# Optimization experiments

Measured on AMD Instinct MI355X. Metric: run time of the kernel, lower is better.

Reference implementation:

```python
import jax, jax.numpy as jnp
import numpy as np

NUM_NODES = 200000
NUM_EDGES = 4000000
NUM_GRAPHS = 512
D = 20
OUT = 5


def setup_inputs() -> dict:
    key = jax.random.key(0)
    k1, k2, k3, k4, k5, k6, k7 = jax.random.split(key, 7)
    x = jax.random.normal(k1, (NUM_NODES, D), dtype=jnp.float32)
    edge_index = jax.random.randint(k2, (2, NUM_EDGES), 0, NUM_NODES, dtype=jnp.int64)
    batch = jnp.sort(jax.random.randint(k3, (NUM_NODES,), 0, NUM_GRAPHS, dtype=jnp.int64))
    # GCNConv weight (glorot-ish) and bias; Linear(20 -> 5) weight/bias
    W1 = jax.random.normal(k4, (D, D), dtype=jnp.float32) / np.sqrt(D)
    b1 = jnp.zeros((D,), dtype=jnp.float32)
    W_out = jax.random.normal(k5, (D, OUT), dtype=jnp.float32) / np.sqrt(D)
    b_out = jax.random.normal(k6, (OUT,), dtype=jnp.float32) * 0.01
    return {"x": x, "edge_index": edge_index, "batch": batch,
            "W1": W1, "b1": b1, "W_out": W_out, "b_out": b_out}


def gcn_conv(x, edge_index, W, b, num_nodes):
    # PyG GCNConv: add self-loops, symmetric norm, linear transform, scatter-add, bias
    loop = jnp.arange(num_nodes, dtype=edge_index.dtype)
    src = jnp.concatenate([edge_index[0], loop])
    dst = jnp.concatenate([edge_index[1], loop])
    deg = jax.ops.segment_sum(jnp.ones_like(dst, dtype=x.dtype), dst, num_segments=num_nodes)
    dinv = jnp.where(deg > 0, jax.lax.rsqrt(deg), 0.0)
    norm = dinv[src] * dinv[dst]  # [E+N]
    h = x @ W                      # [N, D] transform first (cheaper than per-edge)
    msg = h[src] * norm[:, None]   # gather + scale  [E+N, D]
    out = jax.ops.segment_sum(msg, dst, num_segments=num_nodes)  # scatter-add
    return out + b


def reference(x, edge_index, batch, W1, b1, W_out, b_out):
    h = gcn_conv(x, edge_index, W1, b1, NUM_NODES)
    h = jax.nn.relu(h)
    # global mean pool per graph
    sums = jax.ops.segment_sum(h, batch, num_segments=NUM_GRAPHS)          # [G, D]
    cnts = jax.ops.segment_sum(jnp.ones((h.shape[0],), h.dtype), batch, num_segments=NUM_GRAPHS)
    pooled = sums / jnp.maximum(cnts, 1.0)[:, None]
    logits = pooled @ W_out + b_out                                        # [G, 5]
    return jax.nn.softmax(logits, axis=-1)
```

## Files before the change

kernel.cpp:

```cpp
#include <hip/hip_runtime.h>
#include <hip/hip_fp16.h>

#define N_NODES 200000
#define N_EDGES 4000000
#define N_GRAPHS 512
#define D 20
#define OUT 5

#define BSH 6
#define BN 64
#define NFB 3125
#define NFBP 3136
#define NCB 49
#define NC 500
#define CHUNK 8000
#define CH2 7168
#define NCH2 13
#define MAX_EB 1792
#define GMAX 8

__launch_bounds__(1024)
__global__ void k_hist(const int* __restrict__ dst, int* __restrict__ hist_g,
                       float* __restrict__ gsum, int* __restrict__ bucket_tot) {
    __shared__ int h[NFBP];
    int t = threadIdx.x;
    if (blockIdx.x == 0) {
        for (int j = t; j < N_GRAPHS * D; j += 1024) gsum[j] = 0.f;
        for (int j = t; j < NFBP; j += 1024) bucket_tot[j] = 0;
    }
    for (int j = t; j < NFBP; j += 1024) h[j] = 0;
    __syncthreads();
    int base = blockIdx.x * CHUNK;
    for (int k = t; k < CHUNK; k += 1024) atomicAdd(&h[dst[base + k] >> BSH], 1);
    __syncthreads();
    for (int j = t; j < NFBP; j += 1024) hist_g[blockIdx.x * NFBP + j] = h[j];
}

__launch_bounds__(256)
__global__ void k_colsum(const int* __restrict__ hist_g, int* __restrict__ bucket_tot) {
    int col = blockIdx.x * 256 + threadIdx.x;
    if (col >= NFBP) return;
    int r0 = blockIdx.y * 50;
    int sum = 0;
    for (int r = r0; r < r0 + 50; r++) sum += hist_g[r * NFBP + col];
    if (sum) atomicAdd(&bucket_tot[col], sum);
}

__launch_bounds__(1024)
__global__ void k_scan_tot(const int* __restrict__ bucket_tot, int* __restrict__ bucket_base,
                           int* __restrict__ fcursor, int* __restrict__ ccursorA) {
    __shared__ int ps[1024];
    int t = threadIdx.x;
    int base = t * 4;
    int loc[4];
    int sum = 0;
    #pragma unroll
    for (int j = 0; j < 4; j++) {
        int idx = base + j;
        int x = (idx < NFBP) ? bucket_tot[idx] : 0;
        loc[j] = sum;
        sum += x;
    }
    ps[t] = sum;
    __syncthreads();
    for (int off = 1; off < 1024; off <<= 1) {
        int a = (t >= off) ? ps[t - off] : 0;
        __syncthreads();
        ps[t] += a;
        __syncthreads();
    }
    int carry = (t > 0) ? ps[t - 1] : 0;
    #pragma unroll
    for (int j = 0; j < 4; j++) {
        int idx = base + j;
        if (idx < NFBP) {
            int v = carry + loc[j];
            bucket_base[idx] = v;
            fcursor[idx] = v;
        }
    }
    __syncthreads();
    if (t < NCB) ccursorA[t] = bucket_base[t << 6];
}

__launch_bounds__(1024)
__global__ void k_partA(const int* __restrict__ src, const int* __restrict__ dst,
                        int* __restrict__ ccursorA, int* __restrict__ ebufA) {
    __shared__ int h[NCB];
    __shared__ int lcur[NCB];
    int t = threadIdx.x, c = blockIdx.x;
    if (t < NCB) h[t] = 0;
    __syncthreads();
    int base = c * CHUNK;
    for (int k = t; k < CHUNK; k += 1024) atomicAdd(&h[dst[base + k] >> 12], 1);
    __syncthreads();
    if (t < NCB) lcur[t] = atomicAdd(&ccursorA[t], h[t]);
    __syncthreads();
    for (int k = t; k < CHUNK; k += 1024) {
        int d = dst[base + k];
        int sv = src[base + k];
        int cb = d >> 12;
        int pos = atomicAdd(&lcur[cb], 1);
        ebufA[pos] = (sv << 12) | (d & 4095);
    }
}

__launch_bounds__(1024)
__global__ void k_partB(const int* __restrict__ ebufA, const int* __restrict__ bucket_base,
                        int* __restrict__ fcursor, int* __restrict__ ebuf) {
    int cb = blockIdx.x, j = blockIdx.y, t = threadIdx.x;
    int cbase = bucket_base[cb << 6];
    int cend_idx = (cb + 1) << 6; if (cend_idx > NFB) cend_idx = NFB;
    int cend = bucket_base[cend_idx];
    int lo = cbase + j * CH2;
    int hi = lo + CH2; if (hi > cend) hi = cend;
    if (lo >= hi) return;
    __shared__ int h[64];
    __shared__ int lcur[64];
    if (t < 64) h[t] = 0;
    __syncthreads();
    for (int k = lo + t; k < hi; k += 1024) atomicAdd(&h[(ebufA[k] >> 6) & 63], 1);
    __syncthreads();
    if (t < 64) lcur[t] = atomicAdd(&fcursor[(cb << 6) + t], h[t]);
    __syncthreads();
    for (int k = lo + t; k < hi; k += 1024) {
        int p = ebufA[k];
        int sb = (p >> 6) & 63;
        int pos = atomicAdd(&lcur[sb], 1);
        ebuf[pos] = ((p >> 12) << 6) | (p & 63);
    }
}

__launch_bounds__(256)
__global__ void k_count_xh(const int* __restrict__ ebuf, const int* __restrict__ bucket_base,
                           const float4* __restrict__ x4, int* __restrict__ offs_g,
                           uint2* __restrict__ xh2) {
    __shared__ int cnt[BN];
    __shared__ int s[BN];
    __shared__ float sdi[BN];
    int b = blockIdx.x, t = threadIdx.x;
    int eb = bucket_base[b], ee = bucket_base[b + 1];
    if (t < BN) cnt[t] = 0;
    __syncthreads();
    for (int k = eb + t; k < ee; k += 256) atomicAdd(&cnt[ebuf[k] & (BN - 1)], 1);
    __syncthreads();
    int nbn = N_NODES - (b << BSH); if (nbn > BN) nbn = BN;
    int v = (t < BN) ? cnt[t] : 0;
    if (t < BN) s[t] = v;
    __syncthreads();
    for (int off = 1; off < BN; off <<= 1) {
        int a = 0;
        if (t < BN && t >= off) a = s[t - off];
        __syncthreads();
        if (t < BN) s[t] += a;
        __syncthreads();
    }
    if (t < nbn) {
        int node = (b << BSH) + t;
        offs_g[node] = eb + s[t] - v;
        sdi[t] = rsqrtf((float)(v + 1));
    }
    __syncthreads();
    int nw = nbn * 5;
    for (int j = t; j < nw; j += 256) {
        int vl = j / 5, q = j - vl * 5;
        int node = (b << BSH) + vl;
        float4 xv = x4[node * 5 + q];
        float di = sdi[vl];
        __half2 h0 = __float22half2_rn(make_float2(xv.x * di, xv.y * di));
        __half2 h1 = __float22half2_rn(make_float2(xv.z * di, xv.w * di));
        uint2 u;
        u.x = *(unsigned int*)&h0;
        u.y = *(unsigned int*)&h1;
        xh2[node * 5 + q] = u;
    }
}

__device__ __forceinline__ void accu(float& ax, float& ay, float& az, float& aw, uint2 m) {
    float2 m0 = __half22float2(*(__half2*)&m.x);
    float2 m1 = __half22float2(*(__half2*)&m.y);
    ax += m0.x; ay += m0.y; az += m1.x; aw += m1.y;
}

__launch_bounds__(256, 8)
__global__ void k_gather_fused(const int* __restrict__ ebuf, const int* __restrict__ bucket_base,
                               const int* __restrict__ offs_g, const uint2* __restrict__ xh2,
                               const int* __restrict__ batch, const float* __restrict__ W1,
                               const float* __restrict__ b1, float* __restrict__ gsum) {
    __shared__ int loff[BN + 1];
    __shared__ int cur[BN];
    __shared__ int lcsr[MAX_EB];
    __shared__ float w[D * D];
    __shared__ float wb[D];
    __shared__ float sagg[BN][21];
    __shared__ float lgsum[GMAX][D];
    int b = blockIdx.x, t = threadIdx.x;
    int eb = bucket_base[b], ee = bucket_base[b + 1];
    int n = ee - eb;
    int nbn = N_NODES - (b << BSH); if (nbn > BN) nbn = BN;

    for (int j = t; j < D * D; j += 256) w[j] = W1[j];
    if (t < D) wb[t] = b1[t];
    if (t < GMAX * D) ((float*)lgsum)[t] = 0.f;
    if (t < nbn) {
        int o = offs_g[(b << BSH) + t] - eb;
        loff[t] = o;
        cur[t] = o;
    }
    if (t == 0) loff[nbn] = n;
    __syncthreads();

    for (int k = t; k < n; k += 256) {
        int p = ebuf[eb + k];
        int pos = atomicAdd(&cur[p & (BN - 1)], 1);
        if (pos < MAX_EB) lcsr[pos] = p >> BSH;
    }
    __syncthreads();

    int nw = nbn * 5;
    for (int j = t; j < nw; j += 256) {
        int vl = j / 5, q = j - vl * 5;
        int node = (b << BSH) + vl;
        float ax = 0.f, ay = 0.f, az = 0.f, aw_ = 0.f;
        float bx = 0.f, by = 0.f, bz = 0.f, bw = 0.f;
        accu(ax, ay, az, aw_, xh2[node * 5 + q]);
        int lo = loff[vl], hi = loff[vl + 1];
        if (hi > MAX_EB) hi = MAX_EB;
        if (lo > MAX_EB) lo = MAX_EB;
        int k = lo;
        for (; k + 16 <= hi; k += 16) {
            int s0 = lcsr[k],      s1 = lcsr[k + 1],  s2 = lcsr[k + 2],  s3 = lcsr[k + 3];
            int s4 = lcsr[k + 4],  s5 = lcsr[k + 5],  s6 = lcsr[k + 6],  s7 = lcsr[k + 7];
            int s8 = lcsr[k + 8],  s9 = lcsr[k + 9],  sa = lcsr[k + 10], sb = lcsr[k + 11];
            int sc = lcsr[k + 12], sd = lcsr[k + 13], se = lcsr[k + 14], sf = lcsr[k + 15];
            uint2 m0 = xh2[s0 * 5 + q];
            uint2 m1 = xh2[s1 * 5 + q];
            uint2 m2 = xh2[s2 * 5 + q];
            uint2 m3 = xh2[s3 * 5 + q];
            uint2 m4 = xh2[s4 * 5 + q];
            uint2 m5 = xh2[s5 * 5 + q];
            uint2 m6 = xh2[s6 * 5 + q];
            uint2 m7 = xh2[s7 * 5 + q];
            uint2 m8 = xh2[s8 * 5 + q];
            uint2 m9 = xh2[s9 * 5 + q];
            uint2 ma = xh2[sa * 5 + q];
            uint2 mb = xh2[sb * 5 + q];
            uint2 mc = xh2[sc * 5 + q];
            uint2 md = xh2[sd * 5 + q];
            uint2 me = xh2[se * 5 + q];
            uint2 mf = xh2[sf * 5 + q];
            accu(ax, ay, az, aw_, m0); accu(bx, by, bz, bw, m1);
            accu(ax, ay, az, aw_, m2); accu(bx, by, bz, bw, m3);
            accu(ax, ay, az, aw_, m4); accu(bx, by, bz, bw, m5);
            accu(ax, ay, az, aw_, m6); accu(bx, by, bz, bw, m7);
            accu(ax, ay, az, aw_, m8); accu(bx, by, bz, bw, m9);
            accu(ax, ay, az, aw_, ma); accu(bx, by, bz, bw, mb);
            accu(ax, ay, az, aw_, mc); accu(bx, by, bz, bw, md);
            accu(ax, ay, az, aw_, me); accu(bx, by, bz, bw, mf);
        }
        for (; k + 8 <= hi; k += 8) {
            int s0 = lcsr[k],     s1 = lcsr[k + 1], s2 = lcsr[k + 2], s3 = lcsr[k + 3];
            int s4 = lcsr[k + 4], s5 = lcsr[k + 5], s6 = lcsr[k + 6], s7 = lcsr[k + 7];
            uint2 m0 = xh2[s0 * 5 + q];
            uint2 m1 = xh2[s1 * 5 + q];
            uint2 m2 = xh2[s2 * 5 + q];
            uint2 m3 = xh2[s3 * 5 + q];
            uint2 m4 = xh2[s4 * 5 + q];
            uint2 m5 = xh2[s5 * 5 + q];
            uint2 m6 = xh2[s6 * 5 + q];
            uint2 m7 = xh2[s7 * 5 + q];
            accu(ax, ay, az, aw_, m0); accu(bx, by, bz, bw, m1);
            accu(ax, ay, az, aw_, m2); accu(bx, by, bz, bw, m3);
            accu(ax, ay, az, aw_, m4); accu(bx, by, bz, bw, m5);
            accu(ax, ay, az, aw_, m6); accu(bx, by, bz, bw, m7);
        }
        for (; k + 4 <= hi; k += 4) {
            int s0 = lcsr[k], s1 = lcsr[k + 1], s2 = lcsr[k + 2], s3 = lcsr[k + 3];
            uint2 m0 = xh2[s0 * 5 + q];
            uint2 m1 = xh2[s1 * 5 + q];
            uint2 m2 = xh2[s2 * 5 + q];
            uint2 m3 = xh2[s3 * 5 + q];
            accu(ax, ay, az, aw_, m0); accu(bx, by, bz, bw, m1);
            accu(ax, ay, az, aw_, m2); accu(bx, by, bz, bw, m3);
        }
        for (; k < hi; k++) accu(ax, ay, az, aw_, xh2[lcsr[k] * 5 + q]);
        sagg[vl][q * 4 + 0] = ax + bx;
        sagg[vl][q * 4 + 1] = ay + by;
        sagg[vl][q * 4 + 2] = az + bz;
        sagg[vl][q * 4 + 3] = aw_ + bw;
    }
    __syncthreads();

    int g0 = batch[b << BSH];
    int glast = batch[(b << BSH) + nbn - 1];
    int gcnt = glast - g0 + 1;

    if (t < nbn) {
        int node = (b << BSH) + t;
        float di = rsqrtf((float)(loff[t + 1] - loff[t] + 1));
        int gi = batch[node] - g0;
        float pre[D];
        #pragma unroll
        for (int d = 0; d < D; d++) pre[d] = sagg[t][d];
        int t20 = t % D;
        bool fits = (gcnt <= GMAX);
        for (int jj = 0; jj < D; jj++) {
            int o = t20 + jj; if (o >= D) o -= D;
            float h = 0.f;
            #pragma unroll
            for (int d = 0; d < D; d++) h = fmaf(pre[d], w[d * D + o], h);
            h = fmaf(h, di, wb[o]);
            h = fmaxf(h, 0.f);
            if (fits) atomicAdd(&lgsum[gi][o], h);
            else atomicAdd(&gsum[(g0 + gi) * D + o], h);
        }
    }
    __syncthreads();
    if (gcnt <= GMAX && t < gcnt * D) {
        atomicAdd(&gsum[(g0 + t / D) * D + (t % D)], lgsum[t / D][t % D]);
    }
}

__launch_bounds__(64)
__global__ void k_head(const float* __restrict__ gsum, const int* __restrict__ batch,
                       const float* __restrict__ W_out, const float* __restrict__ b_out,
                       float* __restrict__ out) {
    __shared__ float wo[D * OUT];
    __shared__ float bo[OUT];
    int t = threadIdx.x;
    for (int j = t; j < D * OUT; j += 64) wo[j] = W_out[j];
    if (t < OUT) bo[t] = b_out[t];
    __syncthreads();
    int g = blockIdx.x * 64 + t;
    if (g >= N_GRAPHS) return;
    auto lb = [&](int key) {
        int lo = 0, hi = N_NODES;
        while (lo < hi) { int mid = (lo + hi) >> 1; if (batch[mid] < key) lo = mid + 1; else hi = mid; }
        return lo;
    };
    int cnt = lb(g + 1) - lb(g);
    float inv = 1.0f / fmaxf((float)cnt, 1.0f);
    float logits[OUT];
    #pragma unroll
    for (int o = 0; o < OUT; o++) logits[o] = bo[o];
    #pragma unroll
    for (int d = 0; d < D; d++) {
        float p = gsum[g * D + d] * inv;
        #pragma unroll
        for (int o = 0; o < OUT; o++) logits[o] = fmaf(p, wo[d * OUT + o], logits[o]);
    }
    float m = logits[0];
    #pragma unroll
    for (int o = 1; o < OUT; o++) m = fmaxf(m, logits[o]);
    float ex[OUT], sum = 0.f;
    #pragma unroll
    for (int o = 0; o < OUT; o++) { ex[o] = __expf(logits[o] - m); sum += ex[o]; }
    float isum = 1.0f / sum;
    #pragma unroll
    for (int o = 0; o < OUT; o++) out[g * OUT + o] = ex[o] * isum;
}

extern "C" void kernel_launch(void* const* d_in, const int* in_sizes, int n_in,
                              void* d_out, int out_size, void* d_ws, size_t ws_size,
                              hipStream_t stream) {
    const float* x     = (const float*)d_in[0];
    const int*   edge  = (const int*)d_in[1];
    const int*   batch = (const int*)d_in[2];
    const float* W1    = (const float*)d_in[3];
    const float* b1    = (const float*)d_in[4];
    const float* W_out = (const float*)d_in[5];
    const float* b_out = (const float*)d_in[6];
    float* out = (float*)d_out;

    const int* src = edge;
    const int* dst = edge + N_EDGES;
    char* ws = (char*)d_ws;

    int*   hist_g      = (int*)(ws);
    int*   bucket_tot  = (int*)(ws + 6272000);
    int*   bucket_base = (int*)(ws + 6284544);
    int*   fcursor     = (int*)(ws + 6297088);
    int*   ccursorA    = (int*)(ws + 6309632);
    float* gsum        = (float*)(ws + 6309888);
    int*   offs_g      = (int*)(ws + 6350848);
    uint2* xh2         = (uint2*)(ws + 7150848);
    int*   ebufA       = (int*)(ws + 15150848);
    int*   ebuf        = (int*)(ws + 31150848);

    k_hist<<<NC, 1024, 0, stream>>>(dst, hist_g, gsum, bucket_tot);
    k_colsum<<<dim3(13, 10), 256, 0, stream>>>(hist_g, bucket_tot);
    k_scan_tot<<<1, 1024, 0, stream>>>(bucket_tot, bucket_base, fcursor, ccursorA);
    k_partA<<<NC, 1024, 0, stream>>>(src, dst, ccursorA, ebufA);
    k_partB<<<dim3(NCB, NCH2), 1024, 0, stream>>>(ebufA, bucket_base, fcursor, ebuf);
    k_count_xh<<<NFB, 256, 0, stream>>>(ebuf, bucket_base, (const float4*)x, offs_g, xh2);
    k_gather_fused<<<NFB, 256, 0, stream>>>(ebuf, bucket_base, offs_g, xh2, batch, W1, b1, gsum);
    k_head<<<(N_GRAPHS + 63) / 64, 64, 0, stream>>>(gsum, batch, W_out, b_out, out);
}
```

Baseline: 151.7 us.

## Split fp16 features into column-plane arrays and gather in three passes

The half-precision scaled features move from an interleaved 5x8-byte-per-node layout into three planar arrays: two with 16-byte rows holding 8 features each, and one with 8-byte rows holding the last 4. The gather kernel now gives each node four threads that split its edge list, with one pass per plane, and reduces the partial sums through shared memory. This gives wider, more cache-friendly loads per edge and spreads work evenly across threads. In exchange each edge index is read three times, the kernel adds extra barriers and shared memory, and occupancy is lowered to 6 blocks. The nbn tail guards are dropped, which is only safe because the node count divides evenly by 64.

```diff
diff --git a/kernel.cpp b/kernel.cpp
--- a/kernel.cpp
+++ b/kernel.cpp
@@ -134,7 +134,8 @@
 __launch_bounds__(256)
 __global__ void k_count_xh(const int* __restrict__ ebuf, const int* __restrict__ bucket_base,
                            const float4* __restrict__ x4, int* __restrict__ offs_g,
-                           uint2* __restrict__ xh2) {
+                           uint4* __restrict__ xhA, uint4* __restrict__ xhB,
+                           uint2* __restrict__ xhC) {
     __shared__ int cnt[BN];
     __shared__ int s[BN];
     __shared__ float sdi[BN];
@@ -144,7 +145,6 @@
     __syncthreads();
     for (int k = eb + t; k < ee; k += 256) atomicAdd(&cnt[ebuf[k] & (BN - 1)], 1);
     __syncthreads();
-    int nbn = N_NODES - (b << BSH); if (nbn > BN) nbn = BN;
     int v = (t < BN) ? cnt[t] : 0;
     if (t < BN) s[t] = v;
     __syncthreads();
@@ -155,36 +155,57 @@
         if (t < BN) s[t] += a;
         __syncthreads();
     }
-    if (t < nbn) {
+    if (t < BN) {
         int node = (b << BSH) + t;
         offs_g[node] = eb + s[t] - v;
         sdi[t] = rsqrtf((float)(v + 1));
     }
     __syncthreads();
-    int nw = nbn * 5;
-    for (int j = t; j < nw; j += 256) {
-        int vl = j / 5, q = j - vl * 5;
+    for (int j = t; j < BN * 3; j += 256) {
+        int vl = j / 3, q = j - vl * 3;
         int node = (b << BSH) + vl;
-        float4 xv = x4[node * 5 + q];
         float di = sdi[vl];
-        __half2 h0 = __float22half2_rn(make_float2(xv.x * di, xv.y * di));
-        __half2 h1 = __float22half2_rn(make_float2(xv.z * di, xv.w * di));
-        uint2 u;
-        u.x = *(unsigned int*)&h0;
-        u.y = *(unsigned int*)&h1;
-        xh2[node * 5 + q] = u;
-    }
-}
-
-__device__ __forceinline__ void accu(float& ax, float& ay, float& az, float& aw, uint2 m) {
-    float2 m0 = __half22float2(*(__half2*)&m.x);
-    float2 m1 = __half22float2(*(__half2*)&m.y);
-    ax += m0.x; ay += m0.y; az += m1.x; aw += m1.y;
-}
-
-__launch_bounds__(256, 8)
+        if (q < 2) {
+            float4 lo4 = x4[node * 5 + 2 * q];
+            float4 hi4 = x4[node * 5 + 2 * q + 1];
+            __half2 h0 = __float22half2_rn(make_float2(lo4.x * di, lo4.y * di));
+            __half2 h1 = __float22half2_rn(make_float2(lo4.z * di, lo4.w * di));
+            __half2 h2 = __float22half2_rn(make_float2(hi4.x * di, hi4.y * di));
+            __half2 h3 = __float22half2_rn(make_float2(hi4.z * di, hi4.w * di));
+            uint4 u;
+            u.x = *(unsigned int*)&h0; u.y = *(unsigned int*)&h1;
+            u.z = *(unsigned int*)&h2; u.w = *(unsigned int*)&h3;
+            if (q == 0) xhA[node] = u; else xhB[node] = u;
+        } else {
+            float4 lo4 = x4[node * 5 + 4];
+            __half2 h0 = __float22half2_rn(make_float2(lo4.x * di, lo4.y * di));
+            __half2 h1 = __float22half2_rn(make_float2(lo4.z * di, lo4.w * di));
+            uint2 u;
+            u.x = *(unsigned int*)&h0; u.y = *(unsigned int*)&h1;
+            xhC[node] = u;
+        }
+    }
+}
+
+__device__ __forceinline__ void adds8(float& a0, float& a1, float& a2, float& a3,
+                                      float& a4, float& a5, float& a6, float& a7, uint4 m) {
+    float2 f0 = __half22float2(*(__half2*)&m.x);
+    float2 f1 = __half22float2(*(__half2*)&m.y);
+    float2 f2 = __half22float2(*(__half2*)&m.z);
+    float2 f3 = __half22float2(*(__half2*)&m.w);
+    a0 += f0.x; a1 += f0.y; a2 += f1.x; a3 += f1.y;
+    a4 += f2.x; a5 += f2.y; a6 += f3.x; a7 += f3.y;
+}
+__device__ __forceinline__ void adds4(float& a0, float& a1, float& a2, float& a3, uint2 m) {
+    float2 f0 = __half22float2(*(__half2*)&m.x);
+    float2 f1 = __half22float2(*(__half2*)&m.y);
+    a0 += f0.x; a1 += f0.y; a2 += f1.x; a3 += f1.y;
+}
+
+__launch_bounds__(256, 6)
 __global__ void k_gather_fused(const int* __restrict__ ebuf, const int* __restrict__ bucket_base,
-                               const int* __restrict__ offs_g, const uint2* __restrict__ xh2,
+                               const int* __restrict__ offs_g, const uint4* __restrict__ xhA,
+                               const uint4* __restrict__ xhB, const uint2* __restrict__ xhC,
                                const int* __restrict__ batch, const float* __restrict__ W1,
                                const float* __restrict__ b1, float* __restrict__ gsum) {
     __shared__ int loff[BN + 1];
@@ -193,21 +214,21 @@
     __shared__ float w[D * D];
     __shared__ float wb[D];
     __shared__ float sagg[BN][21];
+    __shared__ float part[4][BN][9];
     __shared__ float lgsum[GMAX][D];
     int b = blockIdx.x, t = threadIdx.x;
     int eb = bucket_base[b], ee = bucket_base[b + 1];
     int n = ee - eb;
-    int nbn = N_NODES - (b << BSH); if (nbn > BN) nbn = BN;
 
     for (int j = t; j < D * D; j += 256) w[j] = W1[j];
     if (t < D) wb[t] = b1[t];
     if (t < GMAX * D) ((float*)lgsum)[t] = 0.f;
-    if (t < nbn) {
+    if (t < BN) {
         int o = offs_g[(b << BSH) + t] - eb;
         loff[t] = o;
         cur[t] = o;
     }
-    if (t == 0) loff[nbn] = n;
+    if (t == 0) loff[BN] = n;
     __syncthreads();
 
     for (int k = t; k < n; k += 256) {
@@ -217,88 +238,97 @@
     }
     __syncthreads();
 
-    int nw = nbn * 5;
-    for (int j = t; j < nw; j += 256) {
-        int vl = j / 5, q = j - vl * 5;
-        int node = (b << BSH) + vl;
-        float ax = 0.f, ay = 0.f, az = 0.f, aw_ = 0.f;
-        float bx = 0.f, by = 0.f, bz = 0.f, bw = 0.f;
-        accu(ax, ay, az, aw_, xh2[node * 5 + q]);
-        int lo = loff[vl], hi = loff[vl + 1];
-        if (hi > MAX_EB) hi = MAX_EB;
-        if (lo > MAX_EB) lo = MAX_EB;
-        int k = lo;
-        for (; k + 16 <= hi; k += 16) {
-            int s0 = lcsr[k],      s1 = lcsr[k + 1],  s2 = lcsr[k + 2],  s3 = lcsr[k + 3];
-            int s4 = lcsr[k + 4],  s5 = lcsr[k + 5],  s6 = lcsr[k + 6],  s7 = lcsr[k + 7];
-            int s8 = lcsr[k + 8],  s9 = lcsr[k + 9],  sa = lcsr[k + 10], sb = lcsr[k + 11];
-            int sc = lcsr[k + 12], sd = lcsr[k + 13], se = lcsr[k + 14], sf = lcsr[k + 15];
-            uint2 m0 = xh2[s0 * 5 + q];
-            uint2 m1 = xh2[s1 * 5 + q];
-            uint2 m2 = xh2[s2 * 5 + q];
-            uint2 m3 = xh2[s3 * 5 + q];
-            uint2 m4 = xh2[s4 * 5 + q];
-            uint2 m5 = xh2[s5 * 5 + q];
-            uint2 m6 = xh2[s6 * 5 + q];
-            uint2 m7 = xh2[s7 * 5 + q];
-            uint2 m8 = xh2[s8 * 5 + q];
-            uint2 m9 = xh2[s9 * 5 + q];
-            uint2 ma = xh2[sa * 5 + q];
-            uint2 mb = xh2[sb * 5 + q];
-            uint2 mc = xh2[sc * 5 + q];
-            uint2 md = xh2[sd * 5 + q];
-            uint2 me = xh2[se * 5 + q];
-            uint2 mf = xh2[sf * 5 + q];
-            accu(ax, ay, az, aw_, m0); accu(bx, by, bz, bw, m1);
-            accu(ax, ay, az, aw_, m2); accu(bx, by, bz, bw, m3);
-            accu(ax, ay, az, aw_, m4); accu(bx, by, bz, bw, m5);
-            accu(ax, ay, az, aw_, m6); accu(bx, by, bz, bw, m7);
-            accu(ax, ay, az, aw_, m8); accu(bx, by, bz, bw, m9);
-            accu(ax, ay, az, aw_, ma); accu(bx, by, bz, bw, mb);
-            accu(ax, ay, az, aw_, mc); accu(bx, by, bz, bw, md);
-            accu(ax, ay, az, aw_, me); accu(bx, by, bz, bw, mf);
-        }
-        for (; k + 8 <= hi; k += 8) {
-            int s0 = lcsr[k],     s1 = lcsr[k + 1], s2 = lcsr[k + 2], s3 = lcsr[k + 3];
-            int s4 = lcsr[k + 4], s5 = lcsr[k + 5], s6 = lcsr[k + 6], s7 = lcsr[k + 7];
-            uint2 m0 = xh2[s0 * 5 + q];
-            uint2 m1 = xh2[s1 * 5 + q];
-            uint2 m2 = xh2[s2 * 5 + q];
-            uint2 m3 = xh2[s3 * 5 + q];
-            uint2 m4 = xh2[s4 * 5 + q];
-            uint2 m5 = xh2[s5 * 5 + q];
-            uint2 m6 = xh2[s6 * 5 + q];
-            uint2 m7 = xh2[s7 * 5 + q];
-            accu(ax, ay, az, aw_, m0); accu(bx, by, bz, bw, m1);
-            accu(ax, ay, az, aw_, m2); accu(bx, by, bz, bw, m3);
-            accu(ax, ay, az, aw_, m4); accu(bx, by, bz, bw, m5);
-            accu(ax, ay, az, aw_, m6); accu(bx, by, bz, bw, m7);
-        }
-        for (; k + 4 <= hi; k += 4) {
-            int s0 = lcsr[k], s1 = lcsr[k + 1], s2 = lcsr[k + 2], s3 = lcsr[k + 3];
-            uint2 m0 = xh2[s0 * 5 + q];
-            uint2 m1 = xh2[s1 * 5 + q];
-            uint2 m2 = xh2[s2 * 5 + q];
-            uint2 m3 = xh2[s3 * 5 + q];
-            accu(ax, ay, az, aw_, m0); accu(bx, by, bz, bw, m1);
-            accu(ax, ay, az, aw_, m2); accu(bx, by, bz, bw, m3);
-        }
-        for (; k < hi; k++) accu(ax, ay, az, aw_, xh2[lcsr[k] * 5 + q]);
-        sagg[vl][q * 4 + 0] = ax + bx;
-        sagg[vl][q * 4 + 1] = ay + by;
-        sagg[vl][q * 4 + 2] = az + bz;
-        sagg[vl][q * 4 + 3] = aw_ + bw;
+    int vl = t & 63;
+    int sg = t >> 6;
+    int node = (b << BSH) + vl;
+    int lo0 = loff[vl], hi0 = loff[vl + 1];
+    if (hi0 > MAX_EB) hi0 = MAX_EB;
+    if (lo0 > MAX_EB) lo0 = MAX_EB;
+
+    {
+        float a0=0,a1=0,a2=0,a3=0,a4=0,a5=0,a6=0,a7=0;
+        if (sg == 0) adds8(a0,a1,a2,a3,a4,a5,a6,a7, xhA[node]);
+        int k = lo0 + sg;
+        for (; k + 12 < hi0; k += 16) {
+            int s0 = lcsr[k], s1 = lcsr[k + 4], s2 = lcsr[k + 8], s3 = lcsr[k + 12];
+            uint4 m0 = xhA[s0];
+            uint4 m1 = xhA[s1];
+            uint4 m2 = xhA[s2];
+            uint4 m3 = xhA[s3];
+            adds8(a0,a1,a2,a3,a4,a5,a6,a7, m0);
+            adds8(a0,a1,a2,a3,a4,a5,a6,a7, m1);
+            adds8(a0,a1,a2,a3,a4,a5,a6,a7, m2);
+            adds8(a0,a1,a2,a3,a4,a5,a6,a7, m3);
+        }
+        for (; k < hi0; k += 4) adds8(a0,a1,a2,a3,a4,a5,a6,a7, xhA[lcsr[k]]);
+        part[sg][vl][0]=a0; part[sg][vl][1]=a1; part[sg][vl][2]=a2; part[sg][vl][3]=a3;
+        part[sg][vl][4]=a4; part[sg][vl][5]=a5; part[sg][vl][6]=a6; part[sg][vl][7]=a7;
+    }
+    __syncthreads();
+    for (int j = t; j < BN * 8; j += 256) {
+        int d = j & 7, v = j >> 3;
+        sagg[v][d] = part[0][v][d] + part[1][v][d] + part[2][v][d] + part[3][v][d];
+    }
+    __syncthreads();
+
+    {
+        float a0=0,a1=0,a2=0,a3=0,a4=0,a5=0,a6=0,a7=0;
+        if (sg == 0) adds8(a0,a1,a2,a3,a4,a5,a6,a7, xhB[node]);
+        int k = lo0 + sg;
+        for (; k + 12 < hi0; k += 16) {
+            int s0 = lcsr[k], s1 = lcsr[k + 4], s2 = lcsr[k + 8], s3 = lcsr[k + 12];
+            uint4 m0 = xhB[s0];
+            uint4 m1 = xhB[s1];
+            uint4 m2 = xhB[s2];
+            uint4 m3 = xhB[s3];
+            adds8(a0,a1,a2,a3,a4,a5,a6,a7, m0);
+            adds8(a0,a1,a2,a3,a4,a5,a6,a7, m1);
+            adds8(a0,a1,a2,a3,a4,a5,a6,a7, m2);
+            adds8(a0,a1,a2,a3,a4,a5,a6,a7, m3);
+        }
+        for (; k < hi0; k += 4) adds8(a0,a1,a2,a3,a4,a5,a6,a7, xhB[lcsr[k]]);
+        part[sg][vl][0]=a0; part[sg][vl][1]=a1; part[sg][vl][2]=a2; part[sg][vl][3]=a3;
+        part[sg][vl][4]=a4; part[sg][vl][5]=a5; part[sg][vl][6]=a6; part[sg][vl][7]=a7;
+    }
+    __syncthreads();
+    for (int j = t; j < BN * 8; j += 256) {
+        int d = j & 7, v = j >> 3;
+        sagg[v][8 + d] = part[0][v][d] + part[1][v][d] + part[2][v][d] + part[3][v][d];
+    }
+    __syncthreads();
+
+    {
+        float c0=0,c1=0,c2=0,c3=0;
+        if (sg == 0) adds4(c0,c1,c2,c3, xhC[node]);
+        int k = lo0 + sg;
+        for (; k + 12 < hi0; k += 16) {
+            int s0 = lcsr[k], s1 = lcsr[k + 4], s2 = lcsr[k + 8], s3 = lcsr[k + 12];
+            uint2 m0 = xhC[s0];
+            uint2 m1 = xhC[s1];
+            uint2 m2 = xhC[s2];
+            uint2 m3 = xhC[s3];
+            adds4(c0,c1,c2,c3, m0);
+            adds4(c0,c1,c2,c3, m1);
+            adds4(c0,c1,c2,c3, m2);
+            adds4(c0,c1,c2,c3, m3);
+        }
+        for (; k < hi0; k += 4) adds4(c0,c1,c2,c3, xhC[lcsr[k]]);
+        part[sg][vl][0]=c0; part[sg][vl][1]=c1; part[sg][vl][2]=c2; part[sg][vl][3]=c3;
+    }
+    __syncthreads();
+    for (int j = t; j < BN * 4; j += 256) {
+        int d = j & 3, v = j >> 2;
+        sagg[v][16 + d] = part[0][v][d] + part[1][v][d] + part[2][v][d] + part[3][v][d];
     }
     __syncthreads();
 
     int g0 = batch[b << BSH];
-    int glast = batch[(b << BSH) + nbn - 1];
+    int glast = batch[(b << BSH) + BN - 1];
     int gcnt = glast - g0 + 1;
 
-    if (t < nbn) {
-        int node = (b << BSH) + t;
+    if (t < BN) {
         float di = rsqrtf((float)(loff[t + 1] - loff[t] + 1));
-        int gi = batch[node] - g0;
+        int gi = batch[(b << BSH) + t] - g0;
         float pre[D];
         #pragma unroll
         for (int d = 0; d < D; d++) pre[d] = sagg[t][d];
@@ -383,7 +413,9 @@
     int*   ccursorA    = (int*)(ws + 6309632);
     float* gsum        = (float*)(ws + 6309888);
     int*   offs_g      = (int*)(ws + 6350848);
-    uint2* xh2         = (uint2*)(ws + 7150848);
+    uint4* xhA         = (uint4*)(ws + 7150848);
+    uint4* xhB         = (uint4*)(ws + 10350848);
+    uint2* xhC         = (uint2*)(ws + 13550848);
     int*   ebufA       = (int*)(ws + 15150848);
     int*   ebuf        = (int*)(ws + 31150848);
 
@@ -392,7 +424,9 @@
     k_scan_tot<<<1, 1024, 0, stream>>>(bucket_tot, bucket_base, fcursor, ccursorA);
     k_partA<<<NC, 1024, 0, stream>>>(src, dst, ccursorA, ebufA);
     k_partB<<<dim3(NCB, NCH2), 1024, 0, stream>>>(ebufA, bucket_base, fcursor, ebuf);
-    k_count_xh<<<NFB, 256, 0, stream>>>(ebuf, bucket_base, (const float4*)x, offs_g, xh2);
-    k_gather_fused<<<NFB, 256, 0, stream>>>(ebuf, bucket_base, offs_g, xh2, batch, W1, b1, gsum);
+    k_count_xh<<<NFB, 256, 0, stream>>>(ebuf, bucket_base, (const float4*)x, offs_g,
+                                        xhA, xhB, xhC);
+    k_gather_fused<<<NFB, 256, 0, stream>>>(ebuf, bucket_base, offs_g, xhA, xhB, xhC,
+                                            batch, W1, b1, gsum);
     k_head<<<(N_GRAPHS + 63) / 64, 64, 0, stream>>>(gsum, batch, W_out, b_out, out);
 }
```

Result: slower. 181.1 us (+19.4%).

## Split edge buckets by source half and gather in two passes for locality

Applied to the files above, without the earlier changes.

Each destination bucket is now keyed by whether the source node falls in the lower or upper half of the node range. Aggregation then runs in two passes: one that gathers only lower-half sources and writes partial sums, and one that gathers upper-half sources and finishes the transform and pooling. The goal is to shrink the working set of the random xh2 gather in each pass so it stays cache-resident. The cost is an extra launch, an fp32 partial-aggregate round trip through global memory, a second CSR build per bucket, a larger histogram and scan, and 320-thread blocks with one thread per node feature slot.

```diff
diff --git a/kernel.cpp b/kernel.cpp
--- a/kernel.cpp
+++ b/kernel.cpp
@@ -11,53 +11,59 @@
 #define BN 64
 #define NFB 3125
 #define NFBP 3136
+#define NKEY 6272
 #define NCB 49
 #define NC 500
 #define CHUNK 8000
+#define NCH 250
+#define CHUNK2 16000
 #define CH2 7168
 #define NCH2 13
-#define MAX_EB 1792
+#define HALF 100000
+#define MAX_EBH 1152
 #define GMAX 8
 
 __launch_bounds__(1024)
-__global__ void k_hist(const int* __restrict__ dst, int* __restrict__ hist_g,
-                       float* __restrict__ gsum, int* __restrict__ bucket_tot) {
-    __shared__ int h[NFBP];
+__global__ void k_hist2(const int* __restrict__ src, const int* __restrict__ dst,
+                        int* __restrict__ hist_g, float* __restrict__ gsum) {
+    __shared__ int h[NKEY];
     int t = threadIdx.x;
     if (blockIdx.x == 0) {
         for (int j = t; j < N_GRAPHS * D; j += 1024) gsum[j] = 0.f;
-        for (int j = t; j < NFBP; j += 1024) bucket_tot[j] = 0;
-    }
-    for (int j = t; j < NFBP; j += 1024) h[j] = 0;
-    __syncthreads();
-    int base = blockIdx.x * CHUNK;
-    for (int k = t; k < CHUNK; k += 1024) atomicAdd(&h[dst[base + k] >> BSH], 1);
-    __syncthreads();
-    for (int j = t; j < NFBP; j += 1024) hist_g[blockIdx.x * NFBP + j] = h[j];
+    }
+    for (int j = t; j < NKEY; j += 1024) h[j] = 0;
+    __syncthreads();
+    int base = blockIdx.x * CHUNK2;
+    for (int k = t; k < CHUNK2; k += 1024) {
+        int d = dst[base + k];
+        int s = src[base + k];
+        atomicAdd(&h[((d >> BSH) << 1) | (s >= HALF)], 1);
+    }
+    __syncthreads();
+    for (int j = t; j < NKEY; j += 1024) hist_g[blockIdx.x * NKEY + j] = h[j];
 }
 
 __launch_bounds__(256)
-__global__ void k_colsum(const int* __restrict__ hist_g, int* __restrict__ bucket_tot) {
+__global__ void k_colsum(const int* __restrict__ hist_g, int* __restrict__ btot2) {
     int col = blockIdx.x * 256 + threadIdx.x;
-    if (col >= NFBP) return;
-    int r0 = blockIdx.y * 50;
+    if (col >= NKEY) return;
     int sum = 0;
-    for (int r = r0; r < r0 + 50; r++) sum += hist_g[r * NFBP + col];
-    if (sum) atomicAdd(&bucket_tot[col], sum);
+    for (int r = 0; r < NCH; r++) sum += hist_g[r * NKEY + col];
+    btot2[col] = sum;
 }
 
 __launch_bounds__(1024)
-__global__ void k_scan_tot(const int* __restrict__ bucket_tot, int* __restrict__ bucket_base,
+__global__ void k_scan_tot(const int* __restrict__ btot2, int* __restrict__ bb2,
                            int* __restrict__ fcursor, int* __restrict__ ccursorA) {
     __shared__ int ps[1024];
     int t = threadIdx.x;
-    int base = t * 4;
-    int loc[4];
+    int base = t * 8;
+    int loc[8];
     int sum = 0;
     #pragma unroll
-    for (int j = 0; j < 4; j++) {
+    for (int j = 0; j < 8; j++) {
         int idx = base + j;
-        int x = (idx < NFBP) ? bucket_tot[idx] : 0;
+        int x = (idx < NKEY) ? btot2[idx] : 0;
         loc[j] = sum;
         sum += x;
     }
@@ -71,16 +77,17 @@
     }
     int carry = (t > 0) ? ps[t - 1] : 0;
     #pragma unroll
-    for (int j = 0; j < 4; j++) {
+    for (int j = 0; j < 8; j++) {
         int idx = base + j;
-        if (idx < NFBP) {
+        if (idx < NKEY) {
             int v = carry + loc[j];
-            bucket_base[idx] = v;
+            bb2[idx] = v;
             fcursor[idx] = v;
         }
     }
-    __syncthreads();
-    if (t < NCB) ccursorA[t] = bucket_base[t << 6];
+    if (t == 0) bb2[NKEY] = N_EDGES;
+    __syncthreads();
+    if (t < NCB) ccursorA[t] = bb2[t << 7];
 }
 
 __launch_bounds__(1024)
@@ -106,63 +113,55 @@
 }
 
 __launch_bounds__(1024)
-__global__ void k_partB(const int* __restrict__ ebufA, const int* __restrict__ bucket_base,
+__global__ void k_partB(const int* __restrict__ ebufA, const int* __restrict__ bb2,
                         int* __restrict__ fcursor, int* __restrict__ ebuf) {
     int cb = blockIdx.x, j = blockIdx.y, t = threadIdx.x;
-    int cbase = bucket_base[cb << 6];
+    int cbase = bb2[cb << 7];
     int cend_idx = (cb + 1) << 6; if (cend_idx > NFB) cend_idx = NFB;
-    int cend = bucket_base[cend_idx];
+    int cend = bb2[cend_idx << 1];
     int lo = cbase + j * CH2;
     int hi = lo + CH2; if (hi > cend) hi = cend;
     if (lo >= hi) return;
-    __shared__ int h[64];
-    __shared__ int lcur[64];
-    if (t < 64) h[t] = 0;
-    __syncthreads();
-    for (int k = lo + t; k < hi; k += 1024) atomicAdd(&h[(ebufA[k] >> 6) & 63], 1);
-    __syncthreads();
-    if (t < 64) lcur[t] = atomicAdd(&fcursor[(cb << 6) + t], h[t]);
+    __shared__ int h[128];
+    __shared__ int lcur[128];
+    if (t < 128) h[t] = 0;
     __syncthreads();
     for (int k = lo + t; k < hi; k += 1024) {
         int p = ebufA[k];
-        int sb = (p >> 6) & 63;
-        int pos = atomicAdd(&lcur[sb], 1);
+        int kk = (((p >> 6) & 63) << 1) | ((p >> 12) >= HALF);
+        atomicAdd(&h[kk], 1);
+    }
+    __syncthreads();
+    if (t < 128) lcur[t] = atomicAdd(&fcursor[(cb << 7) + t], h[t]);
+    __syncthreads();
+    for (int k = lo + t; k < hi; k += 1024) {
+        int p = ebufA[k];
+        int kk = (((p >> 6) & 63) << 1) | ((p >> 12) >= HALF);
+        int pos = atomicAdd(&lcur[kk], 1);
         ebuf[pos] = ((p >> 12) << 6) | (p & 63);
     }
 }
 
 __launch_bounds__(256)
-__global__ void k_count_xh(const int* __restrict__ ebuf, const int* __restrict__ bucket_base,
-                           const float4* __restrict__ x4, int* __restrict__ offs_g,
-                           uint2* __restrict__ xh2) {
+__global__ void k_deg_xh(const int* __restrict__ ebuf, const int* __restrict__ bb2,
+                         const float4* __restrict__ x4, float* __restrict__ dinv,
+                         uint2* __restrict__ xh2) {
     __shared__ int cnt[BN];
-    __shared__ int s[BN];
     __shared__ float sdi[BN];
     int b = blockIdx.x, t = threadIdx.x;
-    int eb = bucket_base[b], ee = bucket_base[b + 1];
+    int eb = bb2[2 * b], ee = bb2[2 * b + 2];
     if (t < BN) cnt[t] = 0;
     __syncthreads();
     for (int k = eb + t; k < ee; k += 256) atomicAdd(&cnt[ebuf[k] & (BN - 1)], 1);
     __syncthreads();
-    int nbn = N_NODES - (b << BSH); if (nbn > BN) nbn = BN;
-    int v = (t < BN) ? cnt[t] : 0;
-    if (t < BN) s[t] = v;
-    __syncthreads();
-    for (int off = 1; off < BN; off <<= 1) {
-        int a = 0;
-        if (t < BN && t >= off) a = s[t - off];
-        __syncthreads();
-        if (t < BN) s[t] += a;
-        __syncthreads();
-    }
-    if (t < nbn) {
+    if (t < BN) {
         int node = (b << BSH) + t;
-        offs_g[node] = eb + s[t] - v;
-        sdi[t] = rsqrtf((float)(v + 1));
-    }
-    __syncthreads();
-    int nw = nbn * 5;
-    for (int j = t; j < nw; j += 256) {
+        float di = rsqrtf((float)(cnt[t] + 1));
+        sdi[t] = di;
+        dinv[node] = di;
+    }
+    __syncthreads();
+    for (int j = t; j < BN * 5; j += 256) {
         int vl = j / 5, q = j - vl * 5;
         int node = (b << BSH) + vl;
         float4 xv = x4[node * 5 + q];
@@ -182,123 +181,164 @@
     ax += m0.x; ay += m0.y; az += m1.x; aw += m1.y;
 }
 
-__launch_bounds__(256, 8)
-__global__ void k_gather_fused(const int* __restrict__ ebuf, const int* __restrict__ bucket_base,
-                               const int* __restrict__ offs_g, const uint2* __restrict__ xh2,
-                               const int* __restrict__ batch, const float* __restrict__ W1,
-                               const float* __restrict__ b1, float* __restrict__ gsum) {
-    __shared__ int loff[BN + 1];
-    __shared__ int cur[BN];
-    __shared__ int lcsr[MAX_EB];
+__device__ __forceinline__ int build_csr(const int* __restrict__ ebuf, int r0, int r1,
+                                         int* cnt, int* sl, int* loff, int* cur, int* lcsr,
+                                         int t) {
+    int n = r1 - r0;
+    if (t < BN) cnt[t] = 0;
+    __syncthreads();
+    for (int k = r0 + t; k < r1; k += 320) atomicAdd(&cnt[ebuf[k] & (BN - 1)], 1);
+    __syncthreads();
+    int v = (t < BN) ? cnt[t] : 0;
+    if (t < BN) sl[t] = v;
+    __syncthreads();
+    for (int off = 1; off < BN; off <<= 1) {
+        int a = 0;
+        if (t < BN && t >= off) a = sl[t - off];
+        __syncthreads();
+        if (t < BN) sl[t] += a;
+        __syncthreads();
+    }
+    if (t < BN) {
+        loff[t] = sl[t] - v;
+        cur[t] = sl[t] - v;
+    }
+    if (t == 0) loff[BN] = n;
+    __syncthreads();
+    for (int k = r0 + t; k < r1; k += 320) {
+        int e = ebuf[k];
+        int pos = atomicAdd(&cur[e & (BN - 1)], 1);
+        if (pos < MAX_EBH) lcsr[pos] = e >> BSH;
+    }
+    __syncthreads();
+    return n;
+}
+
+__device__ __forceinline__ void gather_run(const uint2* __restrict__ xh2, const int* lcsr,
+                                           int lo, int hi, int q,
+                                           float& ax, float& ay, float& az, float& aw) {
+    float bx = 0.f, by = 0.f, bz = 0.f, bw = 0.f;
+    int k = lo;
+    for (; k + 16 <= hi; k += 16) {
+        int s0 = lcsr[k],      s1 = lcsr[k + 1],  s2 = lcsr[k + 2],  s3 = lcsr[k + 3];
+        int s4 = lcsr[k + 4],  s5 = lcsr[k + 5],  s6 = lcsr[k + 6],  s7 = lcsr[k + 7];
+        int s8 = lcsr[k + 8],  s9 = lcsr[k + 9],  sa = lcsr[k + 10], sb = lcsr[k + 11];
+        int sc = lcsr[k + 12], sd = lcsr[k + 13], se = lcsr[k + 14], sf = lcsr[k + 15];
+        uint2 m0 = xh2[s0 * 5 + q];
+        uint2 m1 = xh2[s1 * 5 + q];
+        uint2 m2 = xh2[s2 * 5 + q];
+        uint2 m3 = xh2[s3 * 5 + q];
+        uint2 m4 = xh2[s4 * 5 + q];
+        uint2 m5 = xh2[s5 * 5 + q];
+        uint2 m6 = xh2[s6 * 5 + q];
+        uint2 m7 = xh2[s7 * 5 + q];
+        uint2 m8 = xh2[s8 * 5 + q];
+        uint2 m9 = xh2[s9 * 5 + q];
+        uint2 ma = xh2[sa * 5 + q];
+        uint2 mb = xh2[sb * 5 + q];
+        uint2 mc = xh2[sc * 5 + q];
+        uint2 md = xh2[sd * 5 + q];
+        uint2 me = xh2[se * 5 + q];
+        uint2 mf = xh2[sf * 5 + q];
+        accu(ax, ay, az, aw, m0); accu(bx, by, bz, bw, m1);
+        accu(ax, ay, az, aw, m2); accu(bx, by, bz, bw, m3);
+        accu(ax, ay, az, aw, m4); accu(bx, by, bz, bw, m5);
+        accu(ax, ay, az, aw, m6); accu(bx, by, bz, bw, m7);
+        accu(ax, ay, az, aw, m8); accu(bx, by, bz, bw, m9);
+        accu(ax, ay, az, aw, ma); accu(bx, by, bz, bw, mb);
+        accu(ax, ay, az, aw, mc); accu(bx, by, bz, bw, md);
+        accu(ax, ay, az, aw, me); accu(bx, by, bz, bw, mf);
+    }
+    for (; k + 8 <= hi; k += 8) {
+        int s0 = lcsr[k],     s1 = lcsr[k + 1], s2 = lcsr[k + 2], s3 = lcsr[k + 3];
+        int s4 = lcsr[k + 4], s5 = lcsr[k + 5], s6 = lcsr[k + 6], s7 = lcsr[k + 7];
+        uint2 m0 = xh2[s0 * 5 + q];
+        uint2 m1 = xh2[s1 * 5 + q];
+        uint2 m2 = xh2[s2 * 5 + q];
+        uint2 m3 = xh2[s3 * 5 + q];
+        uint2 m4 = xh2[s4 * 5 + q];
+        uint2 m5 = xh2[s5 * 5 + q];
+        uint2 m6 = xh2[s6 * 5 + q];
+        uint2 m7 = xh2[s7 * 5 + q];
+        accu(ax, ay, az, aw, m0); accu(bx, by, bz, bw, m1);
+        accu(ax, ay, az, aw, m2); accu(bx, by, bz, bw, m3);
+        accu(ax, ay, az, aw, m4); accu(bx, by, bz, bw, m5);
+        accu(ax, ay, az, aw, m6); accu(bx, by, bz, bw, m7);
+    }
+    for (; k + 4 <= hi; k += 4) {
+        int s0 = lcsr[k], s1 = lcsr[k + 1], s2 = lcsr[k + 2], s3 = lcsr[k + 3];
+        uint2 m0 = xh2[s0 * 5 + q];
+        uint2 m1 = xh2[s1 * 5 + q];
+        uint2 m2 = xh2[s2 * 5 + q];
+        uint2 m3 = xh2[s3 * 5 + q];
+        accu(ax, ay, az, aw, m0); accu(bx, by, bz, bw, m1);
+        accu(ax, ay, az, aw, m2); accu(bx, by, bz, bw, m3);
+    }
+    for (; k < hi; k++) accu(ax, ay, az, aw, xh2[lcsr[k] * 5 + q]);
+    ax += bx; ay += by; az += bz; aw += bw;
+}
+
+__launch_bounds__(320, 6)
+__global__ void k_gatherP1(const int* __restrict__ ebuf, const int* __restrict__ bb2,
+                           const uint2* __restrict__ xh2, float* __restrict__ agg) {
+    __shared__ int cnt[BN], sl[BN], loff[BN + 1], cur[BN];
+    __shared__ int lcsr[MAX_EBH];
+    int b = blockIdx.x, t = threadIdx.x;
+    int r0 = bb2[2 * b], r1 = bb2[2 * b + 1];
+    build_csr(ebuf, r0, r1, cnt, sl, loff, cur, lcsr, t);
+
+    int vl = t / 5, q = t - vl * 5;
+    int node = (b << BSH) + vl;
+    float ax = 0.f, ay = 0.f, az = 0.f, aw = 0.f;
+    accu(ax, ay, az, aw, xh2[node * 5 + q]);
+    int lo = loff[vl], hi = loff[vl + 1];
+    if (hi > MAX_EBH) hi = MAX_EBH;
+    if (lo > MAX_EBH) lo = MAX_EBH;
+    gather_run(xh2, lcsr, lo, hi, q, ax, ay, az, aw);
+    *(float4*)(agg + (size_t)node * 20 + q * 4) = make_float4(ax, ay, az, aw);
+}
+
+__launch_bounds__(320, 6)
+__global__ void k_gatherP2(const int* __restrict__ ebuf, const int* __restrict__ bb2,
+                           const uint2* __restrict__ xh2, const float* __restrict__ agg,
+                           const float* __restrict__ dinv, const int* __restrict__ batch,
+                           const float* __restrict__ W1, const float* __restrict__ b1,
+                           float* __restrict__ gsum) {
+    __shared__ int cnt[BN], sl[BN], loff[BN + 1], cur[BN];
+    __shared__ int lcsr[MAX_EBH];
     __shared__ float w[D * D];
     __shared__ float wb[D];
     __shared__ float sagg[BN][21];
     __shared__ float lgsum[GMAX][D];
     int b = blockIdx.x, t = threadIdx.x;
-    int eb = bucket_base[b], ee = bucket_base[b + 1];
-    int n = ee - eb;
-    int nbn = N_NODES - (b << BSH); if (nbn > BN) nbn = BN;
-
-    for (int j = t; j < D * D; j += 256) w[j] = W1[j];
+    for (int j = t; j < D * D; j += 320) w[j] = W1[j];
     if (t < D) wb[t] = b1[t];
     if (t < GMAX * D) ((float*)lgsum)[t] = 0.f;
-    if (t < nbn) {
-        int o = offs_g[(b << BSH) + t] - eb;
-        loff[t] = o;
-        cur[t] = o;
-    }
-    if (t == 0) loff[nbn] = n;
-    __syncthreads();
-
-    for (int k = t; k < n; k += 256) {
-        int p = ebuf[eb + k];
-        int pos = atomicAdd(&cur[p & (BN - 1)], 1);
-        if (pos < MAX_EB) lcsr[pos] = p >> BSH;
-    }
-    __syncthreads();
-
-    int nw = nbn * 5;
-    for (int j = t; j < nw; j += 256) {
-        int vl = j / 5, q = j - vl * 5;
-        int node = (b << BSH) + vl;
-        float ax = 0.f, ay = 0.f, az = 0.f, aw_ = 0.f;
-        float bx = 0.f, by = 0.f, bz = 0.f, bw = 0.f;
-        accu(ax, ay, az, aw_, xh2[node * 5 + q]);
-        int lo = loff[vl], hi = loff[vl + 1];
-        if (hi > MAX_EB) hi = MAX_EB;
-        if (lo > MAX_EB) lo = MAX_EB;
-        int k = lo;
-        for (; k + 16 <= hi; k += 16) {
-            int s0 = lcsr[k],      s1 = lcsr[k + 1],  s2 = lcsr[k + 2],  s3 = lcsr[k + 3];
-            int s4 = lcsr[k + 4],  s5 = lcsr[k + 5],  s6 = lcsr[k + 6],  s7 = lcsr[k + 7];
-            int s8 = lcsr[k + 8],  s9 = lcsr[k + 9],  sa = lcsr[k + 10], sb = lcsr[k + 11];
-            int sc = lcsr[k + 12], sd = lcsr[k + 13], se = lcsr[k + 14], sf = lcsr[k + 15];
-            uint2 m0 = xh2[s0 * 5 + q];
-            uint2 m1 = xh2[s1 * 5 + q];
-            uint2 m2 = xh2[s2 * 5 + q];
-            uint2 m3 = xh2[s3 * 5 + q];
-            uint2 m4 = xh2[s4 * 5 + q];
-            uint2 m5 = xh2[s5 * 5 + q];
-            uint2 m6 = xh2[s6 * 5 + q];
-            uint2 m7 = xh2[s7 * 5 + q];
-            uint2 m8 = xh2[s8 * 5 + q];
-            uint2 m9 = xh2[s9 * 5 + q];
-            uint2 ma = xh2[sa * 5 + q];
-            uint2 mb = xh2[sb * 5 + q];
-            uint2 mc = xh2[sc * 5 + q];
-            uint2 md = xh2[sd * 5 + q];
-            uint2 me = xh2[se * 5 + q];
-            uint2 mf = xh2[sf * 5 + q];
-            accu(ax, ay, az, aw_, m0); accu(bx, by, bz, bw, m1);
-            accu(ax, ay, az, aw_, m2); accu(bx, by, bz, bw, m3);
-            accu(ax, ay, az, aw_, m4); accu(bx, by, bz, bw, m5);
-            accu(ax, ay, az, aw_, m6); accu(bx, by, bz, bw, m7);
-            accu(ax, ay, az, aw_, m8); accu(bx, by, bz, bw, m9);
-            accu(ax, ay, az, aw_, ma); accu(bx, by, bz, bw, mb);
-            accu(ax, ay, az, aw_, mc); accu(bx, by, bz, bw, md);
-            accu(ax, ay, az, aw_, me); accu(bx, by, bz, bw, mf);
-        }
-        for (; k + 8 <= hi; k += 8) {
-            int s0 = lcsr[k],     s1 = lcsr[k + 1], s2 = lcsr[k + 2], s3 = lcsr[k + 3];
-            int s4 = lcsr[k + 4], s5 = lcsr[k + 5], s6 = lcsr[k + 6], s7 = lcsr[k + 7];
-            uint2 m0 = xh2[s0 * 5 + q];
-            uint2 m1 = xh2[s1 * 5 + q];
-            uint2 m2 = xh2[s2 * 5 + q];
-            uint2 m3 = xh2[s3 * 5 + q];
-            uint2 m4 = xh2[s4 * 5 + q];
-            uint2 m5 = xh2[s5 * 5 + q];
-            uint2 m6 = xh2[s6 * 5 + q];
-            uint2 m7 = xh2[s7 * 5 + q];
-            accu(ax, ay, az, aw_, m0); accu(bx, by, bz, bw, m1);
-            accu(ax, ay, az, aw_, m2); accu(bx, by, bz, bw, m3);
-            accu(ax, ay, az, aw_, m4); accu(bx, by, bz, bw, m5);
-            accu(ax, ay, az, aw_, m6); accu(bx, by, bz, bw, m7);
-        }
-        for (; k + 4 <= hi; k += 4) {
-            int s0 = lcsr[k], s1 = lcsr[k + 1], s2 = lcsr[k + 2], s3 = lcsr[k + 3];
-            uint2 m0 = xh2[s0 * 5 + q];
-            uint2 m1 = xh2[s1 * 5 + q];
-            uint2 m2 = xh2[s2 * 5 + q];
-            uint2 m3 = xh2[s3 * 5 + q];
-            accu(ax, ay, az, aw_, m0); accu(bx, by, bz, bw, m1);
-            accu(ax, ay, az, aw_, m2); accu(bx, by, bz, bw, m3);
-        }
-        for (; k < hi; k++) accu(ax, ay, az, aw_, xh2[lcsr[k] * 5 + q]);
-        sagg[vl][q * 4 + 0] = ax + bx;
-        sagg[vl][q * 4 + 1] = ay + by;
-        sagg[vl][q * 4 + 2] = az + bz;
-        sagg[vl][q * 4 + 3] = aw_ + bw;
-    }
+    int r0 = bb2[2 * b + 1], r1 = bb2[2 * b + 2];
+    build_csr(ebuf, r0, r1, cnt, sl, loff, cur, lcsr, t);
+
+    int vl = t / 5, q = t - vl * 5;
+    int node = (b << BSH) + vl;
+    float ax = 0.f, ay = 0.f, az = 0.f, aw = 0.f;
+    int lo = loff[vl], hi = loff[vl + 1];
+    if (hi > MAX_EBH) hi = MAX_EBH;
+    if (lo > MAX_EBH) lo = MAX_EBH;
+    gather_run(xh2, lcsr, lo, hi, q, ax, ay, az, aw);
+    float4 prev = *(const float4*)(agg + (size_t)node * 20 + q * 4);
+    sagg[vl][q * 4 + 0] = ax + prev.x;
+    sagg[vl][q * 4 + 1] = ay + prev.y;
+    sagg[vl][q * 4 + 2] = az + prev.z;
+    sagg[vl][q * 4 + 3] = aw + prev.w;
     __syncthreads();
 
     int g0 = batch[b << BSH];
-    int glast = batch[(b << BSH) + nbn - 1];
+    int glast = batch[(b << BSH) + BN - 1];
     int gcnt = glast - g0 + 1;
 
-    if (t < nbn) {
-        int node = (b << BSH) + t;
-        float di = rsqrtf((float)(loff[t + 1] - loff[t] + 1));
-        int gi = batch[node] - g0;
+    if (t < BN) {
+        int nd = (b << BSH) + t;
+        float di = dinv[nd];
+        int gi = batch[nd] - g0;
         float pre[D];
         #pragma unroll
         for (int d = 0; d < D; d++) pre[d] = sagg[t][d];
@@ -376,23 +416,25 @@
     const int* dst = edge + N_EDGES;
     char* ws = (char*)d_ws;
 
-    int*   hist_g      = (int*)(ws);
-    int*   bucket_tot  = (int*)(ws + 6272000);
-    int*   bucket_base = (int*)(ws + 6284544);
-    int*   fcursor     = (int*)(ws + 6297088);
-    int*   ccursorA    = (int*)(ws + 6309632);
-    float* gsum        = (float*)(ws + 6309888);
-    int*   offs_g      = (int*)(ws + 6350848);
-    uint2* xh2         = (uint2*)(ws + 7150848);
-    int*   ebufA       = (int*)(ws + 15150848);
-    int*   ebuf        = (int*)(ws + 31150848);
-
-    k_hist<<<NC, 1024, 0, stream>>>(dst, hist_g, gsum, bucket_tot);
-    k_colsum<<<dim3(13, 10), 256, 0, stream>>>(hist_g, bucket_tot);
-    k_scan_tot<<<1, 1024, 0, stream>>>(bucket_tot, bucket_base, fcursor, ccursorA);
+    int*   hist_g   = (int*)(ws);
+    int*   btot2    = (int*)(ws + 6272000);
+    int*   bb2      = (int*)(ws + 6297600);
+    int*   fcursor  = (int*)(ws + 6323200);
+    int*   ccursorA = (int*)(ws + 6348800);
+    float* gsum     = (float*)(ws + 6349056);
+    float* dinv     = (float*)(ws + 6390016);
+    uint2* xh2      = (uint2*)(ws + 7190016);
+    int*   ebufA    = (int*)(ws + 15190016);
+    float* agg      = (float*)(ws + 15190016);
+    int*   ebuf     = (int*)(ws + 31190016);
+
+    k_hist2<<<NCH, 1024, 0, stream>>>(src, dst, hist_g, gsum);
+    k_colsum<<<(NKEY + 255) / 256, 256, 0, stream>>>(hist_g, btot2);
+    k_scan_tot<<<1, 1024, 0, stream>>>(btot2, bb2, fcursor, ccursorA);
     k_partA<<<NC, 1024, 0, stream>>>(src, dst, ccursorA, ebufA);
-    k_partB<<<dim3(NCB, NCH2), 1024, 0, stream>>>(ebufA, bucket_base, fcursor, ebuf);
-    k_count_xh<<<NFB, 256, 0, stream>>>(ebuf, bucket_base, (const float4*)x, offs_g, xh2);
-    k_gather_fused<<<NFB, 256, 0, stream>>>(ebuf, bucket_base, offs_g, xh2, batch, W1, b1, gsum);
+    k_partB<<<dim3(NCB, NCH2), 1024, 0, stream>>>(ebufA, bb2, fcursor, ebuf);
+    k_deg_xh<<<NFB, 256, 0, stream>>>(ebuf, bb2, (const float4*)x, dinv, xh2);
+    k_gatherP1<<<NFB, 320, 0, stream>>>(ebuf, bb2, xh2, agg);
+    k_gatherP2<<<NFB, 320, 0, stream>>>(ebuf, bb2, xh2, agg, dinv, batch, W1, b1, gsum);
     k_head<<<(N_GRAPHS + 63) / 64, 64, 0, stream>>>(gsum, batch, W_out, b_out, out);
 }
```

Result: slower. 200.5 us (+32.2%).
